# Kernel optimization log

Measured on AMD Instinct MI355X. Metric: run time of the kernel, lower is better.

The kernel has to match this reference:

```python
import jax, jax.numpy as jnp
import numpy as np

HEADS = 4
HEAD_DIM = 32  # out_features // heads = 128 // 4


def setup_inputs() -> dict:
    key = jax.random.key(0)
    k1, k2, k3, k4 = jax.random.split(key, 4)
    N, IN_F = 200000, 128
    E = 500  # <= 1000 so no edge subsampling; loop covers min(E,500)=all edges
    x = jax.random.normal(k1, (N, IN_F), dtype=jnp.float32)
    edge_index = jax.random.randint(k2, (2, E), 0, N, dtype=jnp.int64)
    # Linear weight [out=heads*head_dim, in] as in torch nn.Linear
    W = jax.random.normal(k3, (HEADS * HEAD_DIM, IN_F), dtype=jnp.float32) * (1.0 / np.sqrt(IN_F))
    a = jax.random.normal(k4, (HEADS, 2 * HEAD_DIM), dtype=jnp.float32) * 0.1
    return {"x": x, "edge_index": edge_index, "W": W, "a": a}


def reference(x, edge_index, W, a):
    N = x.shape[0]
    h = (x @ W.T).reshape(N, HEADS, HEAD_DIM)  # [N, H, D]
    src, dst = edge_index[0], edge_index[1]
    h_src = h[src]  # [E, H, D]
    h_dst = h[dst]  # [E, H, D]
    edge_h = jnp.concatenate([h_src, h_dst], axis=-1)  # [E, H, 2D]
    attn = jnp.sum(edge_h * a, axis=-1)  # [E, H]
    attn = jax.nn.leaky_relu(attn, negative_slope=0.2)
    # out[dst] += 0.1 * attn * h[src], accumulated over duplicate dst
    out = h.at[dst].add(0.1 * attn[:, :, None] * h_src)
    return out.reshape(N, HEADS * HEAD_DIM)  # dropout is identity in eval
```

## Files before the change

kernel.cpp:

```cpp
#include <hip/hip_runtime.h>
#include <hip/hip_bf16.h>


typedef __attribute__((ext_vector_type(8))) short bf16x8;
typedef __attribute__((ext_vector_type(4))) float f32x4;

#define W_PAD 136

__global__ __launch_bounds__(256, 4) void gat_gemm_kernel(
    const float* __restrict__ x,
    const float* __restrict__ W,
    float* __restrict__ out,
    int N) {
  __shared__ __hip_bfloat16 Ws[128 * W_PAD];

  const int t = threadIdx.x;

  #pragma unroll
  for (int it = 0; it < 16; ++it) {
    int seg = t + it * 256;
    int row = seg >> 5;
    int off = (seg & 31) * 4;
    float4 v = *reinterpret_cast<const float4*>(&W[row * 128 + off]);
    union { ushort4 u4; __hip_bfloat16 h[4]; } wpk;
    wpk.h[0] = __float2bfloat16(v.x);
    wpk.h[1] = __float2bfloat16(v.y);
    wpk.h[2] = __float2bfloat16(v.z);
    wpk.h[3] = __float2bfloat16(v.w);
    *reinterpret_cast<ushort4*>(&Ws[row * W_PAD + off]) = wpk.u4;
  }
  __syncthreads();

  const int wave = t >> 6;
  const int lane = t & 63;
  const int m = lane & 15;
  const int q = lane >> 4;

  for (int sub = 0; sub < 4; ++sub) {
    const long rowbase = (long)blockIdx.x * 256 + sub * 64 + (long)wave * 16;
    if (rowbase >= N) break;

    const float* xrow = x + (rowbase + m) * 128;

    bf16x8 afrag[4];
    #pragma unroll
    for (int s = 0; s < 4; ++s) {
      float4 v0 = *reinterpret_cast<const float4*>(xrow + s * 32 + q * 8);
      float4 v1 = *reinterpret_cast<const float4*>(xrow + s * 32 + q * 8 + 4);
      union { bf16x8 v; __hip_bfloat16 h[8]; } u;
      u.h[0] = __float2bfloat16(v0.x); u.h[1] = __float2bfloat16(v0.y);
      u.h[2] = __float2bfloat16(v0.z); u.h[3] = __float2bfloat16(v0.w);
      u.h[4] = __float2bfloat16(v1.x); u.h[5] = __float2bfloat16(v1.y);
      u.h[6] = __float2bfloat16(v1.z); u.h[7] = __float2bfloat16(v1.w);
      afrag[s] = u.v;
    }

    f32x4 acc[8];
    #pragma unroll
    for (int nt = 0; nt < 8; ++nt) acc[nt] = (f32x4){0.f, 0.f, 0.f, 0.f};

    #pragma unroll
    for (int s = 0; s < 4; ++s) {
      #pragma unroll
      for (int nt = 0; nt < 8; ++nt) {
        bf16x8 bfrag = *reinterpret_cast<const bf16x8*>(
            &Ws[(nt * 16 + m) * W_PAD + s * 32 + q * 8]);
        acc[nt] = __builtin_amdgcn_mfma_f32_16x16x32_bf16(afrag[s], bfrag,
                                                          acc[nt], 0, 0, 0);
      }
    }

    #pragma unroll
    for (int nt = 0; nt < 8; ++nt) {
      #pragma unroll
      for (int r = 0; r < 4; ++r)
        out[(rowbase + q * 4 + r) * 128 + nt * 16 + m] = acc[nt][r];
    }
  }
}

__device__ __forceinline__ int detect_i64(const int* eidx) {
  int or_odd = 0;
  #pragma unroll
  for (int k = 0; k < 16; ++k) or_odd |= eidx[2 * k + 1];
  return or_odd == 0;
}

__global__ __launch_bounds__(128) void gat_edge_attn(
    const int* __restrict__ eidx,
    const float* __restrict__ a,
    const float* __restrict__ h,
    float* __restrict__ contrib,
    int E) {
  const int e = blockIdx.x;
  const int c = threadIdx.x;
  const bool is64 = detect_i64(eidx);
  const int src = is64 ? eidx[2 * e] : eidx[e];
  const int dst = is64 ? eidx[2 * (E + e)] : eidx[E + e];

  const float hs = h[(long)src * 128 + c];
  const float hd = h[(long)dst * 128 + c];

  const int head = c >> 5, d = c & 31;
  float term = a[head * 64 + d] * hs + a[head * 64 + 32 + d] * hd;
  term += __shfl_xor(term, 16);
  term += __shfl_xor(term, 8);
  term += __shfl_xor(term, 4);
  term += __shfl_xor(term, 2);
  term += __shfl_xor(term, 1);
  const float attn = term >= 0.f ? term : 0.2f * term;

  contrib[(long)e * 128 + c] = 0.1f * attn * hs;
}

__global__ __launch_bounds__(128) void gat_edge_scatter(
    const int* __restrict__ eidx,
    const float* __restrict__ contrib,
    float* __restrict__ out,
    int E) {
  const int e = blockIdx.x;
  const int c = threadIdx.x;
  const bool is64 = detect_i64(eidx);
  const int dst = is64 ? eidx[2 * (E + e)] : eidx[E + e];
  atomicAdd(&out[(long)dst * 128 + c], contrib[(long)e * 128 + c]);
}

extern "C" void kernel_launch(void* const* d_in, const int* in_sizes, int n_in,
                              void* d_out, int out_size, void* d_ws, size_t ws_size,
                              hipStream_t stream) {
  const float* x  = (const float*)d_in[0];
  const int* eidx = (const int*)d_in[1];
  const float* W  = (const float*)d_in[2];
  const float* a  = (const float*)d_in[3];
  float* out = (float*)d_out;
  float* contrib = (float*)d_ws;

  const int N = in_sizes[0] / 128;
  const int E = in_sizes[1] / 2;

  const int blocks = (N + 255) / 256;
  gat_gemm_kernel<<<blocks, 256, 0, stream>>>(x, W, out, N);
  gat_edge_attn<<<E, 128, 0, stream>>>(eidx, a, out, contrib, E);
  gat_edge_scatter<<<E, 128, 0, stream>>>(eidx, contrib, out, E);
}
```

Baseline: 207.1 us.

## Keep W fragments in registers for GEMM and fuse edge attention with scatter

The projection GEMM stops staging W in LDS. Each wave now holds bf16 fragments of two 16-column output tiles in registers, processes four 16-row groups per block, and writes results as float4 stores. The edge attention and scatter kernels are merged into one kernel that recomputes h for src and dst directly from x and W in fp32, then atomically adds into out, dropping the workspace round trip and one launch. The cost is that every block re-reads W from cache. The grid also assumes N is a multiple of 64 and has no tail guard.

```diff
diff --git a/kernel.cpp b/kernel.cpp
--- a/kernel.cpp
+++ b/kernel.cpp
@@ -5,77 +5,69 @@
 typedef __attribute__((ext_vector_type(8))) short bf16x8;
 typedef __attribute__((ext_vector_type(4))) float f32x4;
 
-#define W_PAD 136
+__device__ __forceinline__ bf16x8 cvt2frag(float4 v0, float4 v1) {
+  union { bf16x8 v; __hip_bfloat16 h[8]; } u;
+  u.h[0] = __float2bfloat16(v0.x); u.h[1] = __float2bfloat16(v0.y);
+  u.h[2] = __float2bfloat16(v0.z); u.h[3] = __float2bfloat16(v0.w);
+  u.h[4] = __float2bfloat16(v1.x); u.h[5] = __float2bfloat16(v1.y);
+  u.h[6] = __float2bfloat16(v1.z); u.h[7] = __float2bfloat16(v1.w);
+  return u.v;
+}
 
-__global__ __launch_bounds__(256, 4) void gat_gemm_kernel(
+#define ROWGROUPS 4
+
+__global__ __launch_bounds__(256, 5) void gat_gemm_kernel(
     const float* __restrict__ x,
     const float* __restrict__ W,
     float* __restrict__ out,
     int N) {
-  __shared__ __hip_bfloat16 Ws[128 * W_PAD];
-
   const int t = threadIdx.x;
-
-  #pragma unroll
-  for (int it = 0; it < 16; ++it) {
-    int seg = t + it * 256;
-    int row = seg >> 5;
-    int off = (seg & 31) * 4;
-    float4 v = *reinterpret_cast<const float4*>(&W[row * 128 + off]);
-    union { ushort4 u4; __hip_bfloat16 h[4]; } wpk;
-    wpk.h[0] = __float2bfloat16(v.x);
-    wpk.h[1] = __float2bfloat16(v.y);
-    wpk.h[2] = __float2bfloat16(v.z);
-    wpk.h[3] = __float2bfloat16(v.w);
-    *reinterpret_cast<ushort4*>(&Ws[row * W_PAD + off]) = wpk.u4;
-  }
-  __syncthreads();
-
   const int wave = t >> 6;
   const int lane = t & 63;
   const int m = lane & 15;
   const int q = lane >> 4;
 
-  for (int sub = 0; sub < 4; ++sub) {
-    const long rowbase = (long)blockIdx.x * 256 + sub * 64 + (long)wave * 16;
-    if (rowbase >= N) break;
-
-    const float* xrow = x + (rowbase + m) * 128;
-
-    bf16x8 afrag[4];
+  bf16x8 wf[2][4];
+  #pragma unroll
+  for (int l = 0; l < 2; ++l) {
+    const int nt = wave * 2 + l;
+    const float* wp = W + (nt * 16 + m) * 128 + q * 8;
     #pragma unroll
     for (int s = 0; s < 4; ++s) {
-      float4 v0 = *reinterpret_cast<const float4*>(xrow + s * 32 + q * 8);
-      float4 v1 = *reinterpret_cast<const float4*>(xrow + s * 32 + q * 8 + 4);
-      union { bf16x8 v; __hip_bfloat16 h[8]; } u;
-      u.h[0] = __float2bfloat16(v0.x); u.h[1] = __float2bfloat16(v0.y);
-      u.h[2] = __float2bfloat16(v0.z); u.h[3] = __float2bfloat16(v0.w);
-      u.h[4] = __float2bfloat16(v1.x); u.h[5] = __float2bfloat16(v1.y);
-      u.h[6] = __float2bfloat16(v1.z); u.h[7] = __float2bfloat16(v1.w);
-      afrag[s] = u.v;
+      float4 v0 = *reinterpret_cast<const float4*>(wp + s * 32);
+      float4 v1 = *reinterpret_cast<const float4*>(wp + s * 32 + 4);
+      wf[l][s] = cvt2frag(v0, v1);
+    }
+  }
+
+  #pragma unroll
+  for (int g = 0; g < ROWGROUPS; ++g) {
+    const long rowbase = ((long)blockIdx.x * ROWGROUPS + g) * 16;
+    const float* xp = x + (rowbase + m) * 128 + q * 8;
+
+    float4 v[8];
+    #pragma unroll
+    for (int s = 0; s < 4; ++s) {
+      v[2 * s]     = *reinterpret_cast<const float4*>(xp + s * 32);
+      v[2 * s + 1] = *reinterpret_cast<const float4*>(xp + s * 32 + 4);
+    }
+    bf16x8 xf[4];
+    #pragma unroll
+    for (int s = 0; s < 4; ++s) xf[s] = cvt2frag(v[2 * s], v[2 * s + 1]);
+
+    f32x4 acc0 = (f32x4){0.f, 0.f, 0.f, 0.f};
+    f32x4 acc1 = (f32x4){0.f, 0.f, 0.f, 0.f};
+    #pragma unroll
+    for (int s = 0; s < 4; ++s) {
+      acc0 = __builtin_amdgcn_mfma_f32_16x16x32_bf16(wf[0][s], xf[s], acc0, 0, 0, 0);
+      acc1 = __builtin_amdgcn_mfma_f32_16x16x32_bf16(wf[1][s], xf[s], acc1, 0, 0, 0);
     }
 
-    f32x4 acc[8];
-    #pragma unroll
-    for (int nt = 0; nt < 8; ++nt) acc[nt] = (f32x4){0.f, 0.f, 0.f, 0.f};
-
-    #pragma unroll
-    for (int s = 0; s < 4; ++s) {
-      #pragma unroll
-      for (int nt = 0; nt < 8; ++nt) {
-        bf16x8 bfrag = *reinterpret_cast<const bf16x8*>(
-            &Ws[(nt * 16 + m) * W_PAD + s * 32 + q * 8]);
-        acc[nt] = __builtin_amdgcn_mfma_f32_16x16x32_bf16(afrag[s], bfrag,
-                                                          acc[nt], 0, 0, 0);
-      }
-    }
-
-    #pragma unroll
-    for (int nt = 0; nt < 8; ++nt) {
-      #pragma unroll
-      for (int r = 0; r < 4; ++r)
-        out[(rowbase + q * 4 + r) * 128 + nt * 16 + m] = acc[nt][r];
-    }
+    float* op = out + (rowbase + m) * 128;
+    *reinterpret_cast<float4*>(op + (wave * 2 + 0) * 16 + q * 4) =
+        *reinterpret_cast<float4*>(&acc0);
+    *reinterpret_cast<float4*>(op + (wave * 2 + 1) * 16 + q * 4) =
+        *reinterpret_cast<float4*>(&acc1);
   }
 }
 
@@ -86,11 +78,12 @@
   return or_odd == 0;
 }
 
-__global__ __launch_bounds__(128) void gat_edge_attn(
+__global__ __launch_bounds__(128) void gat_edge_kernel(
+    const float* __restrict__ x,
     const int* __restrict__ eidx,
+    const float* __restrict__ W,
     const float* __restrict__ a,
-    const float* __restrict__ h,
-    float* __restrict__ contrib,
+    float* __restrict__ out,
     int E) {
   const int e = blockIdx.x;
   const int c = threadIdx.x;
@@ -98,8 +91,19 @@
   const int src = is64 ? eidx[2 * e] : eidx[e];
   const int dst = is64 ? eidx[2 * (E + e)] : eidx[E + e];
 
-  const float hs = h[(long)src * 128 + c];
-  const float hd = h[(long)dst * 128 + c];
+  const float4* xs = reinterpret_cast<const float4*>(x + (long)src * 128);
+  const float4* xd = reinterpret_cast<const float4*>(x + (long)dst * 128);
+  const float4* wr = reinterpret_cast<const float4*>(W + (long)c * 128);
+
+  float hs = 0.f, hd = 0.f;
+  #pragma unroll 8
+  for (int k = 0; k < 32; ++k) {
+    float4 w = wr[k], s4 = xs[k], d4 = xd[k];
+    hs = fmaf(w.x, s4.x, hs); hs = fmaf(w.y, s4.y, hs);
+    hs = fmaf(w.z, s4.z, hs); hs = fmaf(w.w, s4.w, hs);
+    hd = fmaf(w.x, d4.x, hd); hd = fmaf(w.y, d4.y, hd);
+    hd = fmaf(w.z, d4.z, hd); hd = fmaf(w.w, d4.w, hd);
+  }
 
   const int head = c >> 5, d = c & 31;
   float term = a[head * 64 + d] * hs + a[head * 64 + 32 + d] * hd;
@@ -110,19 +114,7 @@
   term += __shfl_xor(term, 1);
   const float attn = term >= 0.f ? term : 0.2f * term;
 
-  contrib[(long)e * 128 + c] = 0.1f * attn * hs;
-}
-
-__global__ __launch_bounds__(128) void gat_edge_scatter(
-    const int* __restrict__ eidx,
-    const float* __restrict__ contrib,
-    float* __restrict__ out,
-    int E) {
-  const int e = blockIdx.x;
-  const int c = threadIdx.x;
-  const bool is64 = detect_i64(eidx);
-  const int dst = is64 ? eidx[2 * (E + e)] : eidx[E + e];
-  atomicAdd(&out[(long)dst * 128 + c], contrib[(long)e * 128 + c]);
+  atomicAdd(&out[(long)dst * 128 + c], 0.1f * attn * hs);
 }
 
 extern "C" void kernel_launch(void* const* d_in, const int* in_sizes, int n_in,
@@ -133,13 +125,12 @@
   const float* W  = (const float*)d_in[2];
   const float* a  = (const float*)d_in[3];
   float* out = (float*)d_out;
-  float* contrib = (float*)d_ws;
 
   const int N = in_sizes[0] / 128;
   const int E = in_sizes[1] / 2;
 
-  const int blocks = (N + 255) / 256;
-  gat_gemm_kernel<<<blocks, 256, 0, stream>>>(x, W, out, N);
-  gat_edge_attn<<<E, 128, 0, stream>>>(eidx, a, out, contrib, E);
-  gat_edge_scatter<<<E, 128, 0, stream>>>(eidx, contrib, out, E);
+  const int blocks = (N + 64 * ROWGROUPS - 1) / (64 * ROWGROUPS) * ((64 * ROWGROUPS) / (16 * ROWGROUPS));
+  gat_gemm_kernel<<<N / (16 * ROWGROUPS), 256, 0, stream>>>(x, W, out, N);
+  gat_edge_kernel<<<E, 128, 0, stream>>>(x, eidx, W, a, out, E);
+  (void)blocks; (void)d_ws; (void)ws_size; (void)out_size; (void)n_in;
 }
```

Result: slower. 228.7 us (+10.4%).
